# Optimization experiments

Hardware: AMD Instinct MI355X
Metric: run time of the kernel (lower is better)

The kernel has to match this reference:

```python
import jax, jax.numpy as jnp
import numpy as np

B, S, D = 8, 2048, 1024
SCALE = float(np.sqrt(D))  # math.sqrt(d_model)


def setup_inputs() -> dict:
    key = jax.random.key(0)
    ks = jax.random.split(key, 9)
    inv = 1.0 / np.sqrt(D)  # torch Linear default init range scale
    return {
        "q": jax.random.normal(ks[0], (B, S, D), dtype=jnp.float32),
        "k": jax.random.normal(ks[1], (B, S, D), dtype=jnp.float32),
        "v": jax.random.normal(ks[2], (B, S, D), dtype=jnp.float32),
        "att_mask": jnp.zeros((S, S), dtype=jnp.float32),
        "Wq": jax.random.uniform(ks[3], (D, D), jnp.float32, -inv, inv),
        "bq": jax.random.uniform(ks[4], (D,), jnp.float32, -inv, inv),
        "Wk": jax.random.uniform(ks[5], (D, D), jnp.float32, -inv, inv),
        "bk": jax.random.uniform(ks[6], (D,), jnp.float32, -inv, inv),
        "Wv": jax.random.uniform(ks[7], (D, D), jnp.float32, -inv, inv),
        "bv": jax.random.uniform(ks[8], (D,), jnp.float32, -inv, inv),
    }


def reference(q, k, v, att_mask, Wq, bq, Wk, bk, Wv, bv):
    # Linear projections (torch Linear: x @ W.T + b)
    wq = jnp.einsum('bsd,ed->bse', q, Wq) + bq
    wk = jnp.einsum('bsd,ed->bse', k, Wk) + bk
    wv = jnp.einsum('bsd,ed->bse', v, Wv) + bv
    # bmm(wq, wk^T) / sqrt(d_model) + additive mask
    att_score = jnp.einsum('bqd,bkd->bqk', wq, wk) / SCALE + att_mask
    # softmax over keys; dropout is identity (eval mode) for deterministic reference
    att_weight = jax.nn.softmax(att_score, axis=-1)
    return jnp.einsum('bqk,bkd->bqd', att_weight, wv)
```

## Files before the change

### kernel.cpp

```cpp
#include <hip/hip_runtime.h>
#include <hip/hip_bf16.h>
#include <stdint.h>

typedef __bf16 bf16;
typedef __attribute__((ext_vector_type(8))) __bf16 bf16x8;
typedef __attribute__((ext_vector_type(4))) float f32x4;

#define AS1 __attribute__((address_space(1)))
#define AS3 __attribute__((address_space(3)))

__device__ __forceinline__ void async_copy16(const bf16* g, bf16* l) {
    __builtin_amdgcn_global_load_lds((const AS1 void*)g, (AS3 void*)l, 16, 0, 0);
}

__device__ __forceinline__ unsigned int pack2bf(float a, float b) {
    union { bf16 h[2]; unsigned int u; } o;
    o.h[0] = (bf16)a; o.h[1] = (bf16)b;
    return o.u;
}

__device__ __forceinline__ void conv_body(const float* __restrict__ src,
                                          bf16* __restrict__ dst, size_t i) {
    float4 a = ((const float4*)src)[2 * i];
    float4 b = ((const float4*)src)[2 * i + 1];
    uint4 o;
    o.x = pack2bf(a.x, a.y);
    o.y = pack2bf(a.z, a.w);
    o.z = pack2bf(b.x, b.y);
    o.w = pack2bf(b.z, b.w);
    ((uint4*)dst)[i] = o;
}

__launch_bounds__(256)
__global__ void conv_f2b2(const float* __restrict__ s1, bf16* __restrict__ d1,
                          const float* __restrict__ s2, bf16* __restrict__ d2,
                          int nb1) {
    const int b = blockIdx.x;
    if (b < nb1) conv_body(s1, d1, (size_t)b * 256 + threadIdx.x);
    else         conv_body(s2, d2, (size_t)(b - nb1) * 256 + threadIdx.x);
}

template <int EPI>
__launch_bounds__(512, 2)
__global__ void gemm_nt(const bf16* __restrict__ A, const bf16* __restrict__ B,
                        void* __restrict__ Cv, const float* __restrict__ Aux,
                        float* __restrict__ Rs,
                        int M, int N, int K, float scale) {
    __shared__ bf16 lds[65536];

    const int t    = threadIdx.x;
    const int lane = t & 63;
    const int wave = t >> 6;
    const int wm2  = wave >> 2;
    const int wn2  = wave & 3;
    const int quad = lane >> 4;
    const int ln   = lane & 15;
    const int n0   = blockIdx.x * 256;
    const int m0   = blockIdx.y * 256;
    const size_t zb = blockIdx.z;

    A  += zb * (size_t)M * K;
    B  += zb * (size_t)N * K;
    Rs += zb * (size_t)M;

    f32x4 acc[8][4] = {};

    const int CH0 = t, CH1 = t + 512;
    const int r0 = CH0 >> 2, r1 = CH1 >> 2;
    const int p0 = (CH0 & 3) ^ ((r0 >> 1) & 3);
    const int p1 = (CH1 & 3) ^ ((r1 >> 1) & 3);
    const bf16* Ag0 = A + (size_t)(m0 + r0) * K + p0 * 8;
    const bf16* Ag1 = A + (size_t)(m0 + r1) * K + p1 * 8;
    const bf16* Bg0 = B + (size_t)(n0 + r0) * K + p0 * 8;
    const bf16* Bg1 = B + (size_t)(n0 + r1) * K + p1 * 8;
    const int ld0 = CH0 * 8, ld1 = CH1 * 8;

    const int nt = K >> 5;

    auto stage = [&](int T) {
        const int boff = (T & 3) * 16384;
        const int koff = T * 32;
        async_copy16(Ag0 + koff, &lds[boff + ld0]);
        async_copy16(Ag1 + koff, &lds[boff + ld1]);
        async_copy16(Bg0 + koff, &lds[boff + 8192 + ld0]);
        async_copy16(Bg1 + koff, &lds[boff + 8192 + ld1]);
    };

    stage(0); stage(1); stage(2);
    asm volatile("s_waitcnt vmcnt(8)" ::: "memory");
    __builtin_amdgcn_s_barrier();
    asm volatile("" ::: "memory");

    const int rd     = ln * 32 + ((quad ^ ((ln >> 1) & 3)) * 8);
    const int abase0 = wm2 * 4096 + rd;
    const int bbase0 = 8192 + wn2 * 2048 + rd;

    for (int T = 0; T < nt; ++T) {
        const int boff = (T & 3) * 16384;
        if (T + 3 < nt) stage(T + 3);

        const bf16* la = &lds[boff + abase0];
        const bf16* lb = &lds[boff + bbase0];
        bf16x8 af[8], bfr[4];
#pragma unroll
        for (int i = 0; i < 8; ++i) af[i] = *(const bf16x8*)(la + i * 512);
#pragma unroll
        for (int j = 0; j < 4; ++j) bfr[j] = *(const bf16x8*)(lb + j * 512);

        __builtin_amdgcn_s_setprio(1);
#pragma unroll
        for (int i = 0; i < 8; ++i)
#pragma unroll
            for (int j = 0; j < 4; ++j)
                acc[i][j] = __builtin_amdgcn_mfma_f32_16x16x32_bf16(af[i], bfr[j], acc[i][j], 0, 0, 0);
        __builtin_amdgcn_s_setprio(0);

        const int rem = nt - 1 - T;
        if (rem > 0) {
            if (rem >= 3)      asm volatile("s_waitcnt vmcnt(8)" ::: "memory");
            else if (rem == 2) asm volatile("s_waitcnt vmcnt(4)" ::: "memory");
            else               asm volatile("s_waitcnt vmcnt(0)" ::: "memory");
            __builtin_amdgcn_s_barrier();
            asm volatile("" ::: "memory");
        }
    }

    const int rowb = m0 + wm2 * 128 + quad * 4;

    if constexpr (EPI == 0) {
        bf16* C = (bf16*)Cv;
#pragma unroll
        for (int j = 0; j < 4; ++j) {
            const int col = n0 + wn2 * 64 + j * 16 + ln;
            const float bv = Aux[col];
#pragma unroll
            for (int i = 0; i < 8; ++i)
#pragma unroll
                for (int r = 0; r < 4; ++r)
                    C[(size_t)(rowb + i * 16 + r) * N + col] = (bf16)(acc[i][j][r] + bv);
        }
    } else if constexpr (EPI == 1) {
        bf16* C = (bf16*)Cv;
#pragma unroll
        for (int j = 0; j < 4; ++j) {
            const int col = n0 + wn2 * 64 + j * 16 + ln;
            const float bv = Aux[col];
#pragma unroll
            for (int i = 0; i < 8; ++i) {
                const int row_s = rowb + i * 16;
                uint2 pk;
                pk.x = pack2bf(acc[i][j][0] + bv, acc[i][j][1] + bv);
                pk.y = pack2bf(acc[i][j][2] + bv, acc[i][j][3] + bv);
                const size_t dst = ((size_t)(row_s >> 11) * N + col) * 2048 + (row_s & 2047);
                *(uint2*)&C[dst] = pk;
            }
        }
    } else if constexpr (EPI == 2) {
        bf16* C = (bf16*)Cv + zb * (size_t)M * N;
        float rs[8][4];
#pragma unroll
        for (int i = 0; i < 8; ++i)
#pragma unroll
            for (int r = 0; r < 4; ++r) {
                const size_t base = (size_t)(rowb + i * 16 + r) * N;
                float sp = 0.f;
#pragma unroll
                for (int j = 0; j < 4; ++j) {
                    const int col = n0 + wn2 * 64 + j * 16 + ln;
                    const float e = __expf(acc[i][j][r] * scale + Aux[base + col]);
                    C[base + col] = (bf16)e;
                    sp += e;
                }
                rs[i][r] = sp;
            }
#pragma unroll
        for (int st = 1; st < 16; st <<= 1)
#pragma unroll
            for (int i = 0; i < 8; ++i)
#pragma unroll
                for (int r = 0; r < 4; ++r)
                    rs[i][r] += __shfl_xor(rs[i][r], st, 64);
        if (ln == 0) {
#pragma unroll
            for (int i = 0; i < 8; ++i)
#pragma unroll
                for (int r = 0; r < 4; ++r)
                    atomicAdd(&Rs[rowb + i * 16 + r], rs[i][r]);
        }
    } else {
        float* C = (float*)Cv + zb * (size_t)M * N;
#pragma unroll
        for (int i = 0; i < 8; ++i)
#pragma unroll
            for (int r = 0; r < 4; ++r) {
                const int row = rowb + i * 16 + r;
                const float inv = 1.0f / Rs[row];
                const size_t base = (size_t)row * N;
#pragma unroll
                for (int j = 0; j < 4; ++j)
                    C[base + n0 + wn2 * 64 + j * 16 + ln] = acc[i][j][r] * inv;
            }
    }
}

extern "C" void kernel_launch(void* const* d_in, const int* in_sizes, int n_in,
                              void* d_out, int out_size, void* d_ws, size_t ws_size,
                              hipStream_t stream) {
    (void)in_sizes; (void)n_in; (void)out_size; (void)ws_size;
    const float* q    = (const float*)d_in[0];
    const float* k    = (const float*)d_in[1];
    const float* v    = (const float*)d_in[2];
    const float* mask = (const float*)d_in[3];
    const float* Wq   = (const float*)d_in[4];
    const float* bq   = (const float*)d_in[5];
    const float* Wk   = (const float*)d_in[6];
    const float* bk   = (const float*)d_in[7];
    const float* Wv   = (const float*)d_in[8];
    const float* bv   = (const float*)d_in[9];
    float* out = (float*)d_out;

    bf16* ws  = (bf16*)d_ws;
    bf16* wq  = ws;
    bf16* wk  = ws + (size_t)16777216;
    bf16* Sb  = ws + (size_t)33554432;
    bf16* xb  = Sb;
    bf16* Wb  = ws + (size_t)50331648;
    bf16* vb  = wq;
    bf16* wvT = wk;
    bf16* Wvb = (bf16*)d_out;

    float* Rs = (float*)d_in[0] + ((size_t)16777216 - 16384);

    dim3 cblk(256, 1, 1);
    dim3 gblk(512, 1, 1);

    conv_f2b2<<<dim3(8704), cblk, 0, stream>>>(q, xb, Wq, Wb, 8192);
    hipMemsetAsync(Rs, 0, 16384 * sizeof(float), stream);
    gemm_nt<0><<<dim3(4, 64, 1), gblk, 0, stream>>>(xb, Wb, wq, bq, Rs, 16384, 1024, 1024, 1.0f);
    conv_f2b2<<<dim3(8704), cblk, 0, stream>>>(k, xb, Wk, Wb, 8192);
    gemm_nt<0><<<dim3(4, 64, 1), gblk, 0, stream>>>(xb, Wb, wk, bk, Rs, 16384, 1024, 1024, 1.0f);
    gemm_nt<2><<<dim3(8, 8, 8), gblk, 0, stream>>>(wq, wk, Sb, mask, Rs, 2048, 2048, 1024, 0.03125f);
    conv_f2b2<<<dim3(8704), cblk, 0, stream>>>(v, vb, Wv, Wvb, 8192);
    gemm_nt<1><<<dim3(4, 64, 1), gblk, 0, stream>>>(vb, Wvb, wvT, bv, Rs, 16384, 1024, 1024, 1.0f);
    gemm_nt<3><<<dim3(4, 8, 8), gblk, 0, stream>>>(Sb, wvT, out, nullptr, Rs, 2048, 1024, 2048, 1.0f);
}
```

Baseline: 548.4 us.

## Restructure GEMM main loop into ping-pong half-tile stages with finer barriers

Replaces the 4-deep ring of K=32 tiles with a double-buffered K=64 tile split into halves. Each iteration runs four phases, and each phase interleaves LDS fragment reads, issue of the next async global->LDS copy, a barrier, and a 4x4 MFMA block. The aim is to overlap global loads and LDS reads with MFMA work and to cut register pressure by holding only 4 A fragments at a time. In exchange it adds many more barriers per K step and must get the vmcnt accounting right across phases.

```diff
diff --git a/kernel.cpp b/kernel.cpp
--- a/kernel.cpp
+++ b/kernel.cpp
@@ -11,6 +11,17 @@
 
 __device__ __forceinline__ void async_copy16(const bf16* g, bf16* l) {
     __builtin_amdgcn_global_load_lds((const AS1 void*)g, (AS3 void*)l, 16, 0, 0);
+}
+
+__device__ __forceinline__ void barrier_raw() {
+    asm volatile("" ::: "memory");
+    __builtin_amdgcn_s_barrier();
+    asm volatile("" ::: "memory");
+}
+
+__device__ __forceinline__ void wait_lgkm0_fence() {
+    asm volatile("s_waitcnt lgkmcnt(0)" ::: "memory");
+    __builtin_amdgcn_sched_barrier(0);
 }
 
 __device__ __forceinline__ unsigned int pack2bf(float a, float b) {
@@ -67,62 +78,108 @@
 
     const int CH0 = t, CH1 = t + 512;
     const int r0 = CH0 >> 2, r1 = CH1 >> 2;
-    const int p0 = (CH0 & 3) ^ ((r0 >> 1) & 3);
-    const int p1 = (CH1 & 3) ^ ((r1 >> 1) & 3);
-    const bf16* Ag0 = A + (size_t)(m0 + r0) * K + p0 * 8;
-    const bf16* Ag1 = A + (size_t)(m0 + r1) * K + p1 * 8;
-    const bf16* Bg0 = B + (size_t)(n0 + r0) * K + p0 * 8;
-    const bf16* Bg1 = B + (size_t)(n0 + r1) * K + p1 * 8;
+    const int p0 = ((CH0 & 3) ^ ((r0 >> 1) & 3)) * 8;
+    const int p1 = ((CH1 & 3) ^ ((r1 >> 1) & 3)) * 8;
+    const bf16* Ag0 = A + (size_t)(m0 + r0) * K + p0;
+    const bf16* Ag1 = A + (size_t)(m0 + r1) * K + p1;
+    const bf16* Bg0 = B + (size_t)(n0 + r0) * K + p0;
+    const bf16* Bg1 = B + (size_t)(n0 + r1) * K + p1;
     const int ld0 = CH0 * 8, ld1 = CH1 * 8;
 
-    const int nt = K >> 5;
-
-    auto stage = [&](int T) {
-        const int boff = (T & 3) * 16384;
-        const int koff = T * 32;
-        async_copy16(Ag0 + koff, &lds[boff + ld0]);
-        async_copy16(Ag1 + koff, &lds[boff + ld1]);
-        async_copy16(Bg0 + koff, &lds[boff + 8192 + ld0]);
-        async_copy16(Bg1 + koff, &lds[boff + 8192 + ld1]);
+    const int nt = K >> 6;
+
+    auto stageA = [&](int T, int h) {
+        const int ub  = ((T & 1) * 2 + h) * 8192;
+        const int kof = T * 64 + h * 32;
+        async_copy16(Ag0 + kof, &lds[ub + ld0]);
+        async_copy16(Ag1 + kof, &lds[ub + ld1]);
     };
-
-    stage(0); stage(1); stage(2);
+    auto stageB = [&](int T, int h) {
+        const int ub  = 32768 + ((T & 1) * 2 + h) * 8192;
+        const int kof = T * 64 + h * 32;
+        async_copy16(Bg0 + kof, &lds[ub + ld0]);
+        async_copy16(Bg1 + kof, &lds[ub + ld1]);
+    };
+
+    stageA(0, 0); stageB(0, 0); stageA(0, 1); stageB(0, 1); stageA(1, 0); stageB(1, 0);
     asm volatile("s_waitcnt vmcnt(8)" ::: "memory");
-    __builtin_amdgcn_s_barrier();
-    asm volatile("" ::: "memory");
-
-    const int rd     = ln * 32 + ((quad ^ ((ln >> 1) & 3)) * 8);
-    const int abase0 = wm2 * 4096 + rd;
-    const int bbase0 = 8192 + wn2 * 2048 + rd;
+    barrier_raw();
+
+    const int swz = (quad ^ ((ln >> 1) & 3)) * 8;
+    const int rdA = (wm2 * 128 + ln) * 32 + swz;
+    const int rdB = 32768 + (wn2 * 64 + ln) * 32 + swz;
 
     for (int T = 0; T < nt; ++T) {
-        const int boff = (T & 3) * 16384;
-        if (T + 3 < nt) stage(T + 3);
-
-        const bf16* la = &lds[boff + abase0];
-        const bf16* lb = &lds[boff + bbase0];
-        bf16x8 af[8], bfr[4];
-#pragma unroll
-        for (int i = 0; i < 8; ++i) af[i] = *(const bf16x8*)(la + i * 512);
-#pragma unroll
-        for (int j = 0; j < 4; ++j) bfr[j] = *(const bf16x8*)(lb + j * 512);
-
+        const int sb = (T & 1) * 16384;
+        const bf16* la0 = &lds[sb + rdA];
+        const bf16* la1 = &lds[sb + 8192 + rdA];
+        const bf16* lb0 = &lds[sb + rdB];
+        const bf16* lb1 = &lds[sb + 8192 + rdB];
+        bf16x8 a[4], b[4];
+
+#pragma unroll
+        for (int i = 0; i < 4; ++i) a[i] = *(const bf16x8*)(la0 + i * 512);
+#pragma unroll
+        for (int j = 0; j < 4; ++j) b[j] = *(const bf16x8*)(lb0 + j * 512);
+        if (T + 1 < nt) stageA(T + 1, 1);
+        barrier_raw();
+        wait_lgkm0_fence();
         __builtin_amdgcn_s_setprio(1);
 #pragma unroll
-        for (int i = 0; i < 8; ++i)
+        for (int i = 0; i < 4; ++i)
 #pragma unroll
             for (int j = 0; j < 4; ++j)
-                acc[i][j] = __builtin_amdgcn_mfma_f32_16x16x32_bf16(af[i], bfr[j], acc[i][j], 0, 0, 0);
+                acc[i][j] = __builtin_amdgcn_mfma_f32_16x16x32_bf16(a[i], b[j], acc[i][j], 0, 0, 0);
         __builtin_amdgcn_s_setprio(0);
-
-        const int rem = nt - 1 - T;
-        if (rem > 0) {
-            if (rem >= 3)      asm volatile("s_waitcnt vmcnt(8)" ::: "memory");
-            else if (rem == 2) asm volatile("s_waitcnt vmcnt(4)" ::: "memory");
-            else               asm volatile("s_waitcnt vmcnt(0)" ::: "memory");
-            __builtin_amdgcn_s_barrier();
-            asm volatile("" ::: "memory");
-        }
+        barrier_raw();
+
+#pragma unroll
+        for (int i = 0; i < 4; ++i) a[i] = *(const bf16x8*)(la0 + (4 + i) * 512);
+        if (T + 1 < nt) stageB(T + 1, 1);
+        barrier_raw();
+        wait_lgkm0_fence();
+        __builtin_amdgcn_s_setprio(1);
+#pragma unroll
+        for (int i = 0; i < 4; ++i)
+#pragma unroll
+            for (int j = 0; j < 4; ++j)
+                acc[4 + i][j] = __builtin_amdgcn_mfma_f32_16x16x32_bf16(a[i], b[j], acc[4 + i][j], 0, 0, 0);
+        __builtin_amdgcn_s_setprio(0);
+        if (T == nt - 1) asm volatile("s_waitcnt vmcnt(0)" ::: "memory");
+        else             asm volatile("s_waitcnt vmcnt(8)" ::: "memory");
+        barrier_raw();
+
+#pragma unroll
+        for (int i = 0; i < 4; ++i) a[i] = *(const bf16x8*)(la1 + i * 512);
+#pragma unroll
+        for (int j = 0; j < 4; ++j) b[j] = *(const bf16x8*)(lb1 + j * 512);
+        if (T + 2 < nt) stageA(T + 2, 0);
+        barrier_raw();
+        wait_lgkm0_fence();
+        __builtin_amdgcn_s_setprio(1);
+#pragma unroll
+        for (int i = 0; i < 4; ++i)
+#pragma unroll
+            for (int j = 0; j < 4; ++j)
+                acc[i][j] = __builtin_amdgcn_mfma_f32_16x16x32_bf16(a[i], b[j], acc[i][j], 0, 0, 0);
+        __builtin_amdgcn_s_setprio(0);
+        barrier_raw();
+
+#pragma unroll
+        for (int i = 0; i < 4; ++i) a[i] = *(const bf16x8*)(la1 + (4 + i) * 512);
+        if (T + 2 < nt) stageB(T + 2, 0);
+        barrier_raw();
+        wait_lgkm0_fence();
+        __builtin_amdgcn_s_setprio(1);
+#pragma unroll
+        for (int i = 0; i < 4; ++i)
+#pragma unroll
+            for (int j = 0; j < 4; ++j)
+                acc[4 + i][j] = __builtin_amdgcn_mfma_f32_16x16x32_bf16(a[i], b[j], acc[4 + i][j], 0, 0, 0);
+        __builtin_amdgcn_s_setprio(0);
+        if (T < nt - 2)       asm volatile("s_waitcnt vmcnt(8)" ::: "memory");
+        else if (T == nt - 2) asm volatile("s_waitcnt vmcnt(4)" ::: "memory");
+        barrier_raw();
     }
 
     const int rowb = m0 + wm2 * 128 + quad * 4;
```

Measured after the change: 543.0 us. Within noise of the previous version (-1.0%).
